# Kernel optimization log

Hardware: AMD Instinct MI355X
Metric: run time of the kernel (lower is better)

The kernel has to match this reference:

```python
import jax, jax.numpy as jnp
import numpy as np

N = 100000      # nodes
E = 1600000     # edges (avg degree 16)
IN, HID, OUT = 64, 64, 32
R = 8           # relations


def setup_inputs() -> dict:
    key = jax.random.key(0)
    ks = jax.random.split(key, 8)
    s = jnp.float32(0.05)  # weight init scale
    return {
        "feat": jax.random.normal(ks[0], (N, IN), dtype=jnp.float32),
        "src": jax.random.randint(ks[1], (E,), 0, N),
        "dst": jax.random.randint(ks[2], (E,), 0, N),
        "etypes": jax.random.randint(ks[3], (E,), 0, R),
        "W1": jax.random.normal(ks[4], (R, IN, HID), dtype=jnp.float32) * s,
        "Wself1": jax.random.normal(ks[5], (IN, HID), dtype=jnp.float32) * s,
        "b1": jnp.zeros((HID,), jnp.float32),
        "W2": jax.random.normal(ks[6], (R, HID, OUT), dtype=jnp.float32) * s,
        "Wself2": jax.random.normal(ks[7], (HID, OUT), dtype=jnp.float32) * s,
        "b2": jnp.zeros((OUT,), jnp.float32),
    }


def _rel_graph_conv(h, src, dst, etypes, W, Wself, b):
    """RelGraphConv with sum aggregation, self-loop and bias.

    h: [N, din], W: [R, din, dout], Wself: [din, dout], b: [dout].
    """
    n = h.shape[0]
    # Transform all nodes by all relation weights once: [R, N, dout].
    hW = jnp.einsum('nd,rdo->rno', h, W)
    # Per-edge message: relation-specific transform of the source node.
    msg = hW[etypes, src]                                    # [E, dout]
    # Scatter-add messages to destination nodes.
    agg = jax.ops.segment_sum(msg, dst, num_segments=n)      # [N, dout]
    return agg + h @ Wself + b


def reference(feat, src, dst, etypes, W1, Wself1, b1, W2, Wself2, b2):
    x = jax.nn.relu(_rel_graph_conv(feat, src, dst, etypes, W1, Wself1, b1))
    return _rel_graph_conv(x, src, dst, etypes, W2, Wself2, b2)
```

## Files before the change

kernel.cpp:

```cpp
#include <hip/hip_runtime.h>
#include <hip/hip_bf16.h>

typedef __attribute__((ext_vector_type(8))) short short8;
typedef __attribute__((ext_vector_type(4))) float f32x4;

__device__ __forceinline__ unsigned short f2bf(float v) {
    __hip_bfloat16 h = __float2bfloat16(v);
    return *reinterpret_cast<unsigned short*>(&h);
}
__device__ __forceinline__ float bf2f(unsigned short u) {
    union { unsigned int i; float f; } x;
    x.i = (unsigned int)u << 16;
    return x.f;
}

constexpr int MAXB = 2048;

template<int H>
__global__ __launch_bounds__(256) void transpose_w(
    const float* __restrict__ W, const float* __restrict__ Wself,
    unsigned short* __restrict__ Wt, int R)
{
    int i = blockIdx.x * 256 + threadIdx.x;
    int total = (R + 1) * H * 64;
    if (i >= total) return;
    int d = i & 63;
    int hh = i >> 6;
    int r = hh / H, h = hh % H;
    float v = (r < R) ? W[((size_t)r * 64 + d) * H + h]
                      : Wself[(size_t)d * H + h];
    Wt[i] = f2bf(v);
}

template<int H, int RT>
__global__ __launch_bounds__(512) void gemm_rel_mfma(
    const float* __restrict__ A, const unsigned short* __restrict__ Wt,
    const float* __restrict__ bias,
    unsigned short* __restrict__ C, float* __restrict__ Cself,
    int N, int Rrt, int relu)
{
    constexpr int AS = 72;
    __shared__ unsigned short As[64 * AS];
    const int R = RT ? RT : Rrt;
    const int tid = threadIdx.x;
    const int n0 = blockIdx.x * 64;

    #pragma unroll
    for (int i = 0; i < 2; ++i) {
        int lin = tid + i * 512;
        int n = lin >> 4;
        int d4 = (lin & 15) * 4;
        int gn = n0 + n;
        float4 v = make_float4(0.f, 0.f, 0.f, 0.f);
        if (gn < N) v = *(const float4*)&A[(size_t)gn * 64 + d4];
        if (relu) {
            v.x = fmaxf(v.x, 0.f); v.y = fmaxf(v.y, 0.f);
            v.z = fmaxf(v.z, 0.f); v.w = fmaxf(v.w, 0.f);
        }
        ushort4 u;
        u.x = f2bf(v.x); u.y = f2bf(v.y); u.z = f2bf(v.z); u.w = f2bf(v.w);
        *(ushort4*)&As[n * AS + d4] = u;
    }

    const int w = tid >> 6, lane = tid & 63;
    const int m = lane & 15, quad = lane >> 4;
    const int wt = w & 3;
    const int half = w >> 2;
    const int node = n0 + wt * 16 + m;

    __syncthreads();

    short8 afrag[2];
    afrag[0] = *(const short8*)&As[(wt * 16 + m) * AS + 0 * 32 + quad * 8];
    afrag[1] = *(const short8*)&As[(wt * 16 + m) * AS + 1 * 32 + quad * 8];

    constexpr int NT = H / 32;

    auto wptr = [&](int r, int nt, int kc) {
        int colbase = half * (H / 2) + nt * 16;
        return (const short8*)&Wt[((size_t)(r * H + colbase + m)) * 64 + kc * 32 + quad * 8];
    };

    short8 wf0[NT][2], wf1[NT][2];
    #pragma unroll
    for (int nt = 0; nt < NT; ++nt) { wf0[nt][0] = *wptr(0, nt, 0); wf0[nt][1] = *wptr(0, nt, 1); }
    #pragma unroll
    for (int nt = 0; nt < NT; ++nt) { wf1[nt][0] = *wptr(1, nt, 0); wf1[nt][1] = *wptr(1, nt, 1); }

    #pragma unroll
    for (int r = 0; r <= R; ++r) {
        short8 wn[NT][2];
        if (r + 2 <= R) {
            #pragma unroll
            for (int nt = 0; nt < NT; ++nt) {
                wn[nt][0] = *wptr(r + 2, nt, 0);
                wn[nt][1] = *wptr(r + 2, nt, 1);
            }
        }

        f32x4 acc[NT];
        #pragma unroll
        for (int nt = 0; nt < NT; ++nt) {
            acc[nt] = (f32x4){0.f, 0.f, 0.f, 0.f};
            acc[nt] = __builtin_amdgcn_mfma_f32_16x16x32_bf16(wf0[nt][0], afrag[0], acc[nt], 0, 0, 0);
            acc[nt] = __builtin_amdgcn_mfma_f32_16x16x32_bf16(wf0[nt][1], afrag[1], acc[nt], 0, 0, 0);
        }

        if (r < R) {
            #pragma unroll
            for (int nt = 0; nt < NT; ++nt) {
                int colbase = half * (H / 2) + nt * 16;
                if (node < N) {
                    ushort4 u;
                    u.x = f2bf(acc[nt][0]); u.y = f2bf(acc[nt][1]);
                    u.z = f2bf(acc[nt][2]); u.w = f2bf(acc[nt][3]);
                    *(ushort4*)&C[((size_t)r * N + node) * H + colbase + quad * 4] = u;
                }
            }
        } else {
            #pragma unroll
            for (int nt = 0; nt < NT; ++nt) {
                int colbase = half * (H / 2) + nt * 16;
                if (node < N) {
                    float4 bv = *(const float4*)&bias[colbase + quad * 4];
                    float4 o = make_float4(acc[nt][0] + bv.x, acc[nt][1] + bv.y,
                                           acc[nt][2] + bv.z, acc[nt][3] + bv.w);
                    *(float4*)&Cself[(size_t)node * H + colbase + quad * 4] = o;
                }
            }
        }

        #pragma unroll
        for (int nt = 0; nt < NT; ++nt) {
            wf0[nt][0] = wf1[nt][0]; wf0[nt][1] = wf1[nt][1];
            wf1[nt][0] = wn[nt][0];  wf1[nt][1] = wn[nt][1];
        }
    }
}

__global__ __launch_bounds__(256) void zero_int(int* __restrict__ p, int n) {
    int i = blockIdx.x * 256 + threadIdx.x;
    if (i < n) p[i] = 0;
}

__global__ __launch_bounds__(256) void fine_hist(
    const int* __restrict__ dst, int* __restrict__ ghist, int E, int B, int CH)
{
    __shared__ int hist[MAXB];
    const int t = threadIdx.x;
    const int e0 = blockIdx.x * CH, e1 = min(E, e0 + CH);
    for (int i = t; i < B; i += 256) hist[i] = 0;
    __syncthreads();
    for (int e = e0 + t; e < e1; e += 256) atomicAdd(&hist[dst[e] >> 6], 1);
    __syncthreads();
    for (int i = t; i < B; i += 256) {
        int h = hist[i];
        if (h) atomicAdd(&ghist[i], h);
    }
}

__global__ __launch_bounds__(256) void fine_scan(
    const int* __restrict__ ghist, int* __restrict__ bstart,
    int* __restrict__ cursor, int B, int E)
{
    __shared__ int ts[256];
    const int t = threadIdx.x;
    const int PER = (B + 255) / 256;
    int loc[8];
    int s = 0;
    for (int j = 0; j < PER; ++j) {
        int i = t * PER + j;
        loc[j] = (i < B) ? ghist[i] : 0;
        s += loc[j];
    }
    ts[t] = s;
    __syncthreads();
    for (int off = 1; off < 256; off <<= 1) {
        int x = (t >= off) ? ts[t - off] : 0;
        __syncthreads();
        ts[t] += x;
        __syncthreads();
    }
    int run = ts[t] - s;
    for (int j = 0; j < PER; ++j) {
        int i = t * PER + j;
        if (i < B) { bstart[i] = run; cursor[i] = run; }
        run += loc[j];
    }
    if (t == 255) bstart[B] = E;
}

__global__ __launch_bounds__(256) void partition_fine(
    const int* __restrict__ src, const int* __restrict__ dst,
    const int* __restrict__ et, int* __restrict__ cursor,
    int* __restrict__ rec, int E, int N, int B, int CH)
{
    __shared__ int hist[MAXB];
    __shared__ int base[MAXB];
    __shared__ int cnt[MAXB];
    const int t = threadIdx.x;
    const int e0 = blockIdx.x * CH, e1 = min(E, e0 + CH);

    for (int i = t; i < B; i += 256) hist[i] = 0;
    __syncthreads();
    for (int e = e0 + t; e < e1; e += 256) atomicAdd(&hist[dst[e] >> 6], 1);
    __syncthreads();
    for (int i = t; i < B; i += 256) {
        int h = hist[i];
        base[i] = h ? atomicAdd(&cursor[i], h) : 0;
        cnt[i] = 0;
    }
    __syncthreads();
    for (int e = e0 + t; e < e1; e += 256) {
        int d = dst[e];
        int b = d >> 6;
        int pos = base[b] + atomicAdd(&cnt[b], 1);
        rec[pos] = ((et[e] * N + src[e]) << 6) | (d & 63);
    }
}

__global__ __launch_bounds__(256) void bucket_sort(
    const int* __restrict__ bstart, const int* __restrict__ rec,
    int* __restrict__ eidx, int* __restrict__ row_ptr, int N, int E)
{
    __shared__ int hist[64];
    __shared__ int excl[64];
    __shared__ int cur[64];
    const int b = blockIdx.x;
    const int tid = threadIdx.x;
    const int p0 = bstart[b], p1 = bstart[b + 1];

    if (tid < 64) hist[tid] = 0;
    __syncthreads();
    for (int p = p0 + tid; p < p1; p += 256)
        atomicAdd(&hist[rec[p] & 63], 1);
    __syncthreads();
    if (tid == 0) {
        int run = 0;
        #pragma unroll
        for (int i = 0; i < 64; ++i) { excl[i] = run; run += hist[i]; }
    }
    __syncthreads();
    if (tid < 64) {
        cur[tid] = excl[tid];
        int n = b * 64 + tid;
        if (n < N) row_ptr[n] = p0 + excl[tid];
    }
    if (b == 0 && tid == 0) row_ptr[N] = E;
    __syncthreads();
    for (int p = p0 + tid; p < p1; p += 256) {
        int rv = rec[p];
        int pos = p0 + atomicAdd(&cur[rv & 63], 1);
        eidx[pos] = rv >> 6;
    }
}

template<int F>
__global__ __launch_bounds__(256) void agg_csr(
    const unsigned short* __restrict__ hW, const int* __restrict__ row_ptr,
    const int* __restrict__ eidx, float* __restrict__ out, int N)
{
    constexpr int G = 256 / F;
    const int d = blockIdx.x * G + threadIdx.x / F;
    const int lane = threadIdx.x % F;
    if (d >= N) return;
    const int p1 = row_ptr[d + 1];
    int p = row_ptr[d];
    float a0 = 0.f, a1 = 0.f, a2 = 0.f, a3 = 0.f;
    for (; p + 7 < p1; p += 8) {
        int i0 = eidx[p],     i1 = eidx[p + 1], i2 = eidx[p + 2], i3 = eidx[p + 3];
        int i4 = eidx[p + 4], i5 = eidx[p + 5], i6 = eidx[p + 6], i7 = eidx[p + 7];
        a0 += bf2f(hW[(size_t)i0 * F + lane]);
        a1 += bf2f(hW[(size_t)i1 * F + lane]);
        a2 += bf2f(hW[(size_t)i2 * F + lane]);
        a3 += bf2f(hW[(size_t)i3 * F + lane]);
        a0 += bf2f(hW[(size_t)i4 * F + lane]);
        a1 += bf2f(hW[(size_t)i5 * F + lane]);
        a2 += bf2f(hW[(size_t)i6 * F + lane]);
        a3 += bf2f(hW[(size_t)i7 * F + lane]);
    }
    for (; p + 1 < p1; p += 2) {
        int i0 = eidx[p], i1 = eidx[p + 1];
        a0 += bf2f(hW[(size_t)i0 * F + lane]);
        a1 += bf2f(hW[(size_t)i1 * F + lane]);
    }
    if (p < p1) a0 += bf2f(hW[(size_t)eidx[p] * F + lane]);
    out[(size_t)d * F + lane] += (a0 + a1) + (a2 + a3);
}

extern "C" void kernel_launch(void* const* d_in, const int* in_sizes, int n_in,
                              void* d_out, int out_size, void* d_ws, size_t ws_size,
                              hipStream_t stream)
{
    const float* feat = (const float*)d_in[0];
    const int*   src  = (const int*)d_in[1];
    const int*   dst  = (const int*)d_in[2];
    const int*   et   = (const int*)d_in[3];
    const float* W1   = (const float*)d_in[4];
    const float* Ws1  = (const float*)d_in[5];
    const float* b1   = (const float*)d_in[6];
    const float* W2   = (const float*)d_in[7];
    const float* Ws2  = (const float*)d_in[8];
    const float* b2   = (const float*)d_in[9];
    float* out = (float*)d_out;

    const int N = in_sizes[0] / 64;
    const int E = in_sizes[1];
    const int R = in_sizes[4] / (64 * 64);
    const int B = (N + 63) / 64;

    unsigned short* hW  = (unsigned short*)d_ws;
    float* h1      = (float*)(hW + (size_t)R * N * 64);
    unsigned short* Wt1 = (unsigned short*)(h1 + (size_t)N * 64);
    unsigned short* Wt2 = Wt1 + (size_t)(R + 1) * 64 * 64;
    int*   ghist   = (int*)(Wt2 + (size_t)(R + 1) * 32 * 64);
    int*   bstart  = ghist + B;
    int*   cursor  = bstart + (B + 1);
    int*   row_ptr = cursor + B;
    int*   rec     = row_ptr + (N + 1);
    int*   eidx    = rec + E;

    const dim3 blk(256);
    const int nblk64 = (N + 63) / 64;
    const int P  = 128;
    const int CH = (E + P - 1) / P;

    transpose_w<64><<<((R + 1) * 64 * 64 + 255) / 256, blk, 0, stream>>>(W1, Ws1, Wt1, R);
    transpose_w<32><<<((R + 1) * 32 * 64 + 255) / 256, blk, 0, stream>>>(W2, Ws2, Wt2, R);

    zero_int<<<(B + 255) / 256, blk, 0, stream>>>(ghist, B);
    fine_hist<<<P, blk, 0, stream>>>(dst, ghist, E, B, CH);
    fine_scan<<<1, blk, 0, stream>>>(ghist, bstart, cursor, B, E);
    partition_fine<<<P, blk, 0, stream>>>(src, dst, et, cursor, rec, E, N, B, CH);
    bucket_sort<<<B, blk, 0, stream>>>(bstart, rec, eidx, row_ptr, N, E);

    if (R == 8)
        gemm_rel_mfma<64, 8><<<nblk64, 512, 0, stream>>>(feat, Wt1, b1, hW, h1, N, R, 0);
    else
        gemm_rel_mfma<64, 0><<<nblk64, 512, 0, stream>>>(feat, Wt1, b1, hW, h1, N, R, 0);
    agg_csr<64><<<dim3((N + 3) / 4), blk, 0, stream>>>(hW, row_ptr, eidx, h1, N);

    if (R == 8)
        gemm_rel_mfma<32, 8><<<nblk64, 512, 0, stream>>>(h1, Wt2, b2, hW, out, N, R, 1);
    else
        gemm_rel_mfma<32, 0><<<nblk64, 512, 0, stream>>>(h1, Wt2, b2, hW, out, N, R, 1);
    agg_csr<32><<<dim3((N + 7) / 8), blk, 0, stream>>>(hW, row_ptr, eidx, out, N);
}
```

Measured before the change: 394.2 us.

## Store hidden layer in bf16 and gather two bf16 per lane in aggregation

The intermediate hidden activation h1 is now stored as bf16 instead of fp32. The first GEMM writes it as bf16, the first aggregation reads and writes bf16 pairs, and the second GEMM loads bf16 directly. The aggregation kernels are rewritten so each lane loads 32-bit words holding two bf16 values, with half-waves handling alternate edges and a shuffle combining the partial sums. This is meant to cut memory traffic and the number of load instructions in the gather. It adds an extra bf16 rounding of h1, including after accumulation, which lowers precision.

```diff
diff --git a/kernel.cpp b/kernel.cpp
--- a/kernel.cpp
+++ b/kernel.cpp
@@ -32,11 +32,11 @@
     Wt[i] = f2bf(v);
 }
 
-template<int H, int RT>
+template<int H, int RT, bool ABF, bool SBF>
 __global__ __launch_bounds__(512) void gemm_rel_mfma(
-    const float* __restrict__ A, const unsigned short* __restrict__ Wt,
+    const void* __restrict__ Av, const unsigned short* __restrict__ Wt,
     const float* __restrict__ bias,
-    unsigned short* __restrict__ C, float* __restrict__ Cself,
+    unsigned short* __restrict__ C, void* __restrict__ Cselfv,
     int N, int Rrt, int relu)
 {
     constexpr int AS = 72;
@@ -45,21 +45,38 @@
     const int tid = threadIdx.x;
     const int n0 = blockIdx.x * 64;
 
-    #pragma unroll
-    for (int i = 0; i < 2; ++i) {
-        int lin = tid + i * 512;
-        int n = lin >> 4;
-        int d4 = (lin & 15) * 4;
+    if constexpr (ABF) {
+        const unsigned short* A = (const unsigned short*)Av;
+        int n = tid >> 3, d8 = (tid & 7) * 8;
         int gn = n0 + n;
-        float4 v = make_float4(0.f, 0.f, 0.f, 0.f);
-        if (gn < N) v = *(const float4*)&A[(size_t)gn * 64 + d4];
+        short8 u = {};
+        if (gn < N) u = *(const short8*)&A[(size_t)gn * 64 + d8];
         if (relu) {
-            v.x = fmaxf(v.x, 0.f); v.y = fmaxf(v.y, 0.f);
-            v.z = fmaxf(v.z, 0.f); v.w = fmaxf(v.w, 0.f);
-        }
-        ushort4 u;
-        u.x = f2bf(v.x); u.y = f2bf(v.y); u.z = f2bf(v.z); u.w = f2bf(v.w);
-        *(ushort4*)&As[n * AS + d4] = u;
+            #pragma unroll
+            for (int j = 0; j < 8; ++j) {
+                unsigned short x = (unsigned short)u[j];
+                u[j] = (short)((x & 0x8000) ? 0 : x);
+            }
+        }
+        *(short8*)&As[n * AS + d8] = u;
+    } else {
+        const float* A = (const float*)Av;
+        #pragma unroll
+        for (int i = 0; i < 2; ++i) {
+            int lin = tid + i * 512;
+            int n = lin >> 4;
+            int d4 = (lin & 15) * 4;
+            int gn = n0 + n;
+            float4 v = make_float4(0.f, 0.f, 0.f, 0.f);
+            if (gn < N) v = *(const float4*)&A[(size_t)gn * 64 + d4];
+            if (relu) {
+                v.x = fmaxf(v.x, 0.f); v.y = fmaxf(v.y, 0.f);
+                v.z = fmaxf(v.z, 0.f); v.w = fmaxf(v.w, 0.f);
+            }
+            ushort4 u;
+            u.x = f2bf(v.x); u.y = f2bf(v.y); u.z = f2bf(v.z); u.w = f2bf(v.w);
+            *(ushort4*)&As[n * AS + d4] = u;
+        }
     }
 
     const int w = tid >> 6, lane = tid & 63;
@@ -123,9 +140,18 @@
                 int colbase = half * (H / 2) + nt * 16;
                 if (node < N) {
                     float4 bv = *(const float4*)&bias[colbase + quad * 4];
-                    float4 o = make_float4(acc[nt][0] + bv.x, acc[nt][1] + bv.y,
-                                           acc[nt][2] + bv.z, acc[nt][3] + bv.w);
-                    *(float4*)&Cself[(size_t)node * H + colbase + quad * 4] = o;
+                    if constexpr (SBF) {
+                        unsigned short* Cs = (unsigned short*)Cselfv;
+                        ushort4 u;
+                        u.x = f2bf(acc[nt][0] + bv.x); u.y = f2bf(acc[nt][1] + bv.y);
+                        u.z = f2bf(acc[nt][2] + bv.z); u.w = f2bf(acc[nt][3] + bv.w);
+                        *(ushort4*)&Cs[(size_t)node * H + colbase + quad * 4] = u;
+                    } else {
+                        float* Cs = (float*)Cselfv;
+                        float4 o = make_float4(acc[nt][0] + bv.x, acc[nt][1] + bv.y,
+                                               acc[nt][2] + bv.z, acc[nt][3] + bv.w);
+                        *(float4*)&Cs[(size_t)node * H + colbase + quad * 4] = o;
+                    }
                 }
             }
         }
@@ -255,37 +281,77 @@
     }
 }
 
-template<int F>
-__global__ __launch_bounds__(256) void agg_csr(
-    const unsigned short* __restrict__ hW, const int* __restrict__ row_ptr,
+__global__ __launch_bounds__(256) void agg_csr64(
+    const unsigned int* __restrict__ hw32, const int* __restrict__ row_ptr,
+    const int* __restrict__ eidx, unsigned int* __restrict__ out32, int N)
+{
+    const int d = blockIdx.x * 4 + (threadIdx.x >> 6);
+    const int lane = threadIdx.x & 63;
+    if (d >= N) return;
+    const int he = lane >> 5;
+    const int c = lane & 31;
+    const int p0 = row_ptr[d], p1 = row_ptr[d + 1];
+    float s0 = 0.f, s1 = 0.f, t0 = 0.f, t1 = 0.f;
+    int p = p0 + he;
+    for (; p + 6 < p1; p += 8) {
+        unsigned int v0 = hw32[(size_t)eidx[p]     * 32 + c];
+        unsigned int v1 = hw32[(size_t)eidx[p + 2] * 32 + c];
+        unsigned int v2 = hw32[(size_t)eidx[p + 4] * 32 + c];
+        unsigned int v3 = hw32[(size_t)eidx[p + 6] * 32 + c];
+        s0 += bf2f((unsigned short)(v0 & 0xffff)); s1 += bf2f((unsigned short)(v0 >> 16));
+        t0 += bf2f((unsigned short)(v1 & 0xffff)); t1 += bf2f((unsigned short)(v1 >> 16));
+        s0 += bf2f((unsigned short)(v2 & 0xffff)); s1 += bf2f((unsigned short)(v2 >> 16));
+        t0 += bf2f((unsigned short)(v3 & 0xffff)); t1 += bf2f((unsigned short)(v3 >> 16));
+    }
+    for (; p < p1; p += 2) {
+        unsigned int v = hw32[(size_t)eidx[p] * 32 + c];
+        s0 += bf2f((unsigned short)(v & 0xffff)); s1 += bf2f((unsigned short)(v >> 16));
+    }
+    s0 += t0; s1 += t1;
+    float u0 = __shfl(s0, c + 32, 64);
+    float u1 = __shfl(s1, c + 32, 64);
+    if (he == 0) {
+        unsigned int cur = out32[(size_t)d * 32 + c];
+        float o0 = s0 + u0 + bf2f((unsigned short)(cur & 0xffff));
+        float o1 = s1 + u1 + bf2f((unsigned short)(cur >> 16));
+        out32[(size_t)d * 32 + c] = (unsigned int)f2bf(o0) | ((unsigned int)f2bf(o1) << 16);
+    }
+}
+
+__global__ __launch_bounds__(256) void agg_csr32(
+    const unsigned int* __restrict__ hw32, const int* __restrict__ row_ptr,
     const int* __restrict__ eidx, float* __restrict__ out, int N)
 {
-    constexpr int G = 256 / F;
-    const int d = blockIdx.x * G + threadIdx.x / F;
-    const int lane = threadIdx.x % F;
+    const int d = blockIdx.x * 8 + (threadIdx.x >> 5);
+    const int l = threadIdx.x & 31;
     if (d >= N) return;
-    const int p1 = row_ptr[d + 1];
-    int p = row_ptr[d];
-    float a0 = 0.f, a1 = 0.f, a2 = 0.f, a3 = 0.f;
-    for (; p + 7 < p1; p += 8) {
-        int i0 = eidx[p],     i1 = eidx[p + 1], i2 = eidx[p + 2], i3 = eidx[p + 3];
-        int i4 = eidx[p + 4], i5 = eidx[p + 5], i6 = eidx[p + 6], i7 = eidx[p + 7];
-        a0 += bf2f(hW[(size_t)i0 * F + lane]);
-        a1 += bf2f(hW[(size_t)i1 * F + lane]);
-        a2 += bf2f(hW[(size_t)i2 * F + lane]);
-        a3 += bf2f(hW[(size_t)i3 * F + lane]);
-        a0 += bf2f(hW[(size_t)i4 * F + lane]);
-        a1 += bf2f(hW[(size_t)i5 * F + lane]);
-        a2 += bf2f(hW[(size_t)i6 * F + lane]);
-        a3 += bf2f(hW[(size_t)i7 * F + lane]);
-    }
-    for (; p + 1 < p1; p += 2) {
-        int i0 = eidx[p], i1 = eidx[p + 1];
-        a0 += bf2f(hW[(size_t)i0 * F + lane]);
-        a1 += bf2f(hW[(size_t)i1 * F + lane]);
-    }
-    if (p < p1) a0 += bf2f(hW[(size_t)eidx[p] * F + lane]);
-    out[(size_t)d * F + lane] += (a0 + a1) + (a2 + a3);
+    const int he = l >> 4;
+    const int c = l & 15;
+    const int p0 = row_ptr[d], p1 = row_ptr[d + 1];
+    float s0 = 0.f, s1 = 0.f, t0 = 0.f, t1 = 0.f;
+    int p = p0 + he;
+    for (; p + 6 < p1; p += 8) {
+        unsigned int v0 = hw32[(size_t)eidx[p]     * 16 + c];
+        unsigned int v1 = hw32[(size_t)eidx[p + 2] * 16 + c];
+        unsigned int v2 = hw32[(size_t)eidx[p + 4] * 16 + c];
+        unsigned int v3 = hw32[(size_t)eidx[p + 6] * 16 + c];
+        s0 += bf2f((unsigned short)(v0 & 0xffff)); s1 += bf2f((unsigned short)(v0 >> 16));
+        t0 += bf2f((unsigned short)(v1 & 0xffff)); t1 += bf2f((unsigned short)(v1 >> 16));
+        s0 += bf2f((unsigned short)(v2 & 0xffff)); s1 += bf2f((unsigned short)(v2 >> 16));
+        t0 += bf2f((unsigned short)(v3 & 0xffff)); t1 += bf2f((unsigned short)(v3 >> 16));
+    }
+    for (; p < p1; p += 2) {
+        unsigned int v = hw32[(size_t)eidx[p] * 16 + c];
+        s0 += bf2f((unsigned short)(v & 0xffff)); s1 += bf2f((unsigned short)(v >> 16));
+    }
+    s0 += t0; s1 += t1;
+    float u0 = __shfl(s0, (threadIdx.x & 63) ^ 16, 64);
+    float u1 = __shfl(s1, (threadIdx.x & 63) ^ 16, 64);
+    if (he == 0) {
+        float2 cur = *(const float2*)&out[(size_t)d * 32 + c * 2];
+        float2 o = make_float2(cur.x + s0 + u0, cur.y + s1 + u1);
+        *(float2*)&out[(size_t)d * 32 + c * 2] = o;
+    }
 }
 
 extern "C" void kernel_launch(void* const* d_in, const int* in_sizes, int n_in,
@@ -310,8 +376,8 @@
     const int B = (N + 63) / 64;
 
     unsigned short* hW  = (unsigned short*)d_ws;
-    float* h1      = (float*)(hW + (size_t)R * N * 64);
-    unsigned short* Wt1 = (unsigned short*)(h1 + (size_t)N * 64);
+    unsigned short* h1  = hW + (size_t)R * N * 64;
+    unsigned short* Wt1 = h1 + (size_t)N * 64;
     unsigned short* Wt2 = Wt1 + (size_t)(R + 1) * 64 * 64;
     int*   ghist   = (int*)(Wt2 + (size_t)(R + 1) * 32 * 64);
     int*   bstart  = ghist + B;
@@ -335,14 +401,15 @@
     bucket_sort<<<B, blk, 0, stream>>>(bstart, rec, eidx, row_ptr, N, E);
 
     if (R == 8)
-        gemm_rel_mfma<64, 8><<<nblk64, 512, 0, stream>>>(feat, Wt1, b1, hW, h1, N, R, 0);
+        gemm_rel_mfma<64, 8, false, true><<<nblk64, 512, 0, stream>>>(feat, Wt1, b1, hW, h1, N, R, 0);
     else
-        gemm_rel_mfma<64, 0><<<nblk64, 512, 0, stream>>>(feat, Wt1, b1, hW, h1, N, R, 0);
-    agg_csr<64><<<dim3((N + 3) / 4), blk, 0, stream>>>(hW, row_ptr, eidx, h1, N);
+        gemm_rel_mfma<64, 0, false, true><<<nblk64, 512, 0, stream>>>(feat, Wt1, b1, hW, h1, N, R, 0);
+    agg_csr64<<<dim3((N + 3) / 4), blk, 0, stream>>>((const unsigned int*)hW, row_ptr, eidx,
+                                                     (unsigned int*)h1, N);
 
     if (R == 8)
-        gemm_rel_mfma<32, 8><<<nblk64, 512, 0, stream>>>(h1, Wt2, b2, hW, out, N, R, 1);
+        gemm_rel_mfma<32, 8, true, false><<<nblk64, 512, 0, stream>>>(h1, Wt2, b2, hW, out, N, R, 1);
     else
-        gemm_rel_mfma<32, 0><<<nblk64, 512, 0, stream>>>(h1, Wt2, b2, hW, out, N, R, 1);
-    agg_csr<32><<<dim3((N + 7) / 8), blk, 0, stream>>>(hW, row_ptr, eidx, out, N);
-}
+        gemm_rel_mfma<32, 0, true, false><<<nblk64, 512, 0, stream>>>(h1, Wt2, b2, hW, out, N, R, 1);
+    agg_csr32<<<dim3((N + 7) / 8), blk, 0, stream>>>((const unsigned int*)hW, row_ptr, eidx, out, N);
+}
```

After: 375.5 us. 4.7% less time.
